# Optimization experiments

Hardware: AMD Instinct MI355X
Metric: run time of the kernel (lower is better)

## Reference

```python
import jax, jax.numpy as jnp
import numpy as np

DEPTH = 3  # chemprop default message passing depth


def setup_inputs() -> dict:
    key = jax.random.key(0)
    ks = jax.random.split(key, 10)
    n_atoms, n_bonds, max_nb, n_mols = 50000, 100000, 6, 2000
    atom_fdim, bond_fdim, hidden = 133, 147, 300
    f_atoms = jax.random.normal(ks[0], (n_atoms, atom_fdim), dtype=jnp.float32)
    f_bonds = jax.random.normal(ks[1], (n_bonds, bond_fdim), dtype=jnp.float32)
    a2b = jax.random.randint(ks[2], (n_atoms, max_nb), 0, n_bonds, dtype=jnp.int32)
    b2a = jax.random.randint(ks[3], (n_bonds,), 0, n_atoms, dtype=jnp.int32)
    b2revb = jax.random.randint(ks[4], (n_bonds,), 0, n_bonds, dtype=jnp.int32)
    mol_id = jnp.sort(jax.random.randint(ks[5], (n_atoms,), 0, n_mols, dtype=jnp.int32))
    W_i = jax.random.normal(ks[6], (bond_fdim, hidden), dtype=jnp.float32) * 0.05
    W_h = jax.random.normal(ks[7], (hidden, hidden), dtype=jnp.float32) * 0.05
    W_o = jax.random.normal(ks[8], (atom_fdim + hidden, hidden), dtype=jnp.float32) * 0.05
    b_o = jnp.zeros((hidden,), dtype=jnp.float32)
    return {"f_atoms": f_atoms, "f_bonds": f_bonds, "a2b": a2b, "b2a": b2a,
            "b2revb": b2revb, "mol_id": mol_id, "n_mols": n_mols,
            "W_i": W_i, "W_h": W_h, "W_o": W_o, "b_o": b_o}


def reference(f_atoms, f_bonds, a2b, b2a, b2revb, mol_id, n_mols, W_i, W_h, W_o, b_o):
    act = jax.nn.relu
    # W_i: bond features -> hidden; message init
    inp = f_bonds @ W_i                      # [n_bonds, h]
    message = act(inp)
    for _ in range(DEPTH - 1):
        nei = message[a2b]                    # [n_atoms, max_nb, h] gather
        a_message = nei.sum(axis=1)           # [n_atoms, h]
        rev = message[b2revb]                 # [n_bonds, h]
        message = a_message[b2a] - rev        # [n_bonds, h]
        message = act(inp + message @ W_h)
    # final atom readout
    a_message = message[a2b].sum(axis=1)      # [n_atoms, h]
    a_input = jnp.concatenate([f_atoms, a_message], axis=1)  # [n_atoms, fa+h]
    atom_hiddens = act(a_input @ W_o + b_o)   # [n_atoms, h]
    # ragged per-molecule mean (a_scope loop -> segment mean)
    sums = jax.ops.segment_sum(atom_hiddens, mol_id, num_segments=n_mols)
    counts = jax.ops.segment_sum(jnp.ones((atom_hiddens.shape[0],), dtype=atom_hiddens.dtype), mol_id, num_segments=n_mols)
    mol_vecs = jnp.where(counts[:, None] > 0, sums / jnp.maximum(counts, 1.0)[:, None], 0.0)
    return mol_vecs
```

## Files before the change

kernel.cpp:

```cpp
#include <hip/hip_runtime.h>
#include <cstddef>

#define H 300
#define RS 304
#define MAXNB 6
#define ASTR 312

typedef __attribute__((ext_vector_type(8)))  short bf16x8;
typedef __attribute__((ext_vector_type(16))) float f32x16;

__device__ __forceinline__ float bf2f(unsigned short u) {
    return __uint_as_float(((unsigned int)u) << 16);
}
__device__ __forceinline__ unsigned short f2bf(float f) {
    unsigned int u = __float_as_uint(f);
    u += 0x7FFFu + ((u >> 16) & 1u);
    return (unsigned short)(u >> 16);
}
__device__ __forceinline__ unsigned int sub2bf(unsigned int a, unsigned int b) {
    float d0 = bf2f((unsigned short)(a & 0xFFFFu)) - bf2f((unsigned short)(b & 0xFFFFu));
    float d1 = bf2f((unsigned short)(a >> 16))     - bf2f((unsigned short)(b >> 16));
    return (unsigned int)f2bf(d0) | ((unsigned int)f2bf(d1) << 16);
}
__device__ __forceinline__ unsigned int relu2(unsigned int w) {
    unsigned int r = w;
    if (w & 0x80000000u) r &= 0x0000FFFFu;
    if (w & 0x00008000u) r &= 0xFFFF0000u;
    return r;
}
__device__ __forceinline__ uint4 relu4(uint4 v) {
    v.x = relu2(v.x); v.y = relu2(v.y); v.z = relu2(v.z); v.w = relu2(v.w);
    return v;
}
__device__ __forceinline__ uint4 subpack4(uint4 a, uint4 b) {
    uint4 r;
    r.x = sub2bf(a.x, b.x); r.y = sub2bf(a.y, b.y);
    r.z = sub2bf(a.z, b.z); r.w = sub2bf(a.w, b.w);
    return r;
}


template<int S>
__global__ void __launch_bounds__(256)
pack_a_f32_c(const float* __restrict__ src, unsigned short* __restrict__ dst,
             int M, int K)
{
    __shared__ unsigned short sm[64 * 152];
    const int m0 = blockIdx.x * 64;
    const int r = threadIdx.x >> 2;
    const int q = threadIdx.x & 3;
    int mv = m0 + r; if (mv >= M) mv = M - 1;
    const float* rowF = src + (size_t)mv * K;
#pragma unroll
    for (int i = 0; i < (S * 4 + 3) / 4; ++i) {
        int c = q + i * 4;
        if (c * 4 < S * 16) {
            unsigned short h[4];
#pragma unroll
            for (int e = 0; e < 4; ++e) {
                int k = c * 4 + e;
                h[e] = (k < K) ? f2bf(rowF[k]) : (unsigned short)0;
            }
            uint2 o;
            o.x = (unsigned int)h[0] | ((unsigned int)h[1] << 16);
            o.y = (unsigned int)h[2] | ((unsigned int)h[3] << 16);
            *(uint2*)&sm[r * 152 + c * 4] = o;
        }
    }
    __syncthreads();
    for (int j = threadIdx.x; j < 2 * S * 64; j += 256) {
        int lane = j & 63;
        int t = j >> 6;
        int s = t % S;
        int mb2 = t / S;
        uint4 v = *(const uint4*)&sm[(mb2 * 32 + (lane & 31)) * 152 + s * 16 + (lane >> 5) * 8];
        int m_blk = blockIdx.x * 2 + mb2;
        *(uint4*)&dst[((size_t)(m_blk * S + s) * 64 + lane) * 8] = v;
    }
}

__global__ void __launch_bounds__(256)
pack_b(const float* __restrict__ src1, const float* __restrict__ src2,
       unsigned short* __restrict__ dst, int K1, int S1, int K2, int SB)
{
    int g = blockIdx.x * 256 + threadIdx.x;
    if (g >= 10 * SB * 64) return;
    int lane = g & 63;
    int t = g >> 6;
    int s = t % SB;
    int n_blk = t / SB;
    int n = n_blk * 32 + (lane & 31);
    unsigned int w[4];
#pragma unroll
    for (int p = 0; p < 4; ++p) {
        unsigned short h[2];
#pragma unroll
        for (int e = 0; e < 2; ++e) {
            int kf = s * 16 + (lane >> 5) * 8 + p * 2 + e;
            float v = 0.0f;
            if (n < H) {
                if (s < S1) {
                    if (kf < K1) v = src1[(size_t)kf * H + n];
                } else {
                    int k2 = kf - S1 * 16;
                    if (k2 < K2) v = src2[(size_t)k2 * H + n];
                }
            }
            h[e] = f2bf(v);
        }
        w[p] = (unsigned int)h[0] | ((unsigned int)h[1] << 16);
    }
    *(uint4*)&dst[(size_t)g * 8] = make_uint4(w[0], w[1], w[2], w[3]);
}

template<int RELU>
__global__ void __launch_bounds__(256)
aggregate_row(const unsigned short* __restrict__ msg, const int* __restrict__ a2b,
              unsigned short* __restrict__ amsg, int n_atoms)
{
    int gid = blockIdx.x * 256 + threadIdx.x;
    int total = n_atoms * 38;
    if (gid >= total) return;
    int atom = gid / 38;
    int g8 = gid - atom * 38;
    const int* nb = a2b + atom * MAXNB;
    float sum[8] = {};
#pragma unroll
    for (int j = 0; j < MAXNB; ++j) {
        int b = nb[j];
        uint4 v = *(const uint4*)&msg[(size_t)b * RS + g8 * 8];
        if (RELU) v = relu4(v);
        unsigned int ww[4] = {v.x, v.y, v.z, v.w};
#pragma unroll
        for (int p = 0; p < 4; ++p) {
            sum[p * 2]     += bf2f((unsigned short)(ww[p] & 0xFFFFu));
            sum[p * 2 + 1] += bf2f((unsigned short)(ww[p] >> 16));
        }
    }
    unsigned int ow[4];
#pragma unroll
    for (int p = 0; p < 4; ++p)
        ow[p] = (unsigned int)f2bf(sum[p * 2]) | ((unsigned int)f2bf(sum[p * 2 + 1]) << 16);
    *(uint4*)&amsg[(size_t)atom * RS + g8 * 8] = make_uint4(ow[0], ow[1], ow[2], ow[3]);
}

template<int S1, int S2, int SBL, int MODE, int RELUMSG>
__global__ void __launch_bounds__(640)
gemm_fused(const unsigned short* __restrict__ A1,
           const unsigned short* __restrict__ amsg,
           const unsigned short* __restrict__ msg,
           const int* __restrict__ b2a, const int* __restrict__ b2revb,
           const unsigned short* __restrict__ Bp,
           const float* __restrict__ bias,
           const unsigned short* __restrict__ inp_add,
           const float* __restrict__ Adense, int Kd,
           unsigned short* __restrict__ out, int M)
{
    __shared__ __align__(16) unsigned short smem[64 * ASTR];

    const int lane  = threadIdx.x & 63;
    const int w     = threadIdx.x >> 6;
    const int mrow  = lane & 31;
    const int quad  = lane >> 5;
    const int m0    = blockIdx.x * 64;

    if (threadIdx.x < 512) {
        const int r = threadIdx.x >> 3;
        const int q = threadIdx.x & 7;
        int mm = m0 + r;
        int mv = (mm < M) ? mm : 0;
        if (MODE == 0) {
            if (mm >= M) mv = M - 1;
            const float* rowF = Adense + (size_t)mv * Kd;
#pragma unroll
            for (int i = 0; i < 5; ++i) {
                int c = q + i * 8;
                if (c * 4 < S2 * 16) {
                    unsigned short h[4];
#pragma unroll
                    for (int e = 0; e < 4; ++e) {
                        int k = c * 4 + e;
                        h[e] = (k < Kd) ? f2bf(rowF[k]) : (unsigned short)0;
                    }
                    uint2 o;
                    o.x = (unsigned int)h[0] | ((unsigned int)h[1] << 16);
                    o.y = (unsigned int)h[2] | ((unsigned int)h[3] << 16);
                    *(uint2*)&smem[r * ASTR + c * 4] = o;
                }
            }
        } else {
            const unsigned short* rowA;
            const unsigned short* rowM = nullptr;
            if (MODE == 1) {
                rowA = amsg + (size_t)b2a[mv] * RS;
                rowM = msg  + (size_t)b2revb[mv] * RS;
            } else {
                rowA = amsg + (size_t)mv * RS;
            }
#pragma unroll
            for (int i = 0; i < 5; ++i) {
                int c = q + i * 8;
                if (c < 38) {
                    uint4 o;
                    if (MODE == 1) {
                        uint4 va = *(const uint4*)(rowA + c * 8);
                        uint4 vm = *(const uint4*)(rowM + c * 8);
                        if (RELUMSG) vm = relu4(vm);
                        o = subpack4(va, vm);
                    } else {
                        o = *(const uint4*)(rowA + c * 8);
                    }
                    *(uint4*)&smem[r * ASTR + c * 8] = o;
                }
            }
        }
    }
    __syncthreads();

    f32x16 acc_lo, acc_hi;
#pragma unroll
    for (int i = 0; i < 16; ++i) { acc_lo[i] = 0.0f; acc_hi[i] = 0.0f; }

    const unsigned short* pa1_lo = (S1 > 0)
        ? (A1 + ((size_t)(blockIdx.x * 2 + 0) * S1 * 64 + lane) * 8) : nullptr;
    const unsigned short* pa1_hi = (S1 > 0)
        ? (A1 + ((size_t)(blockIdx.x * 2 + 1) * S1 * 64 + lane) * 8) : nullptr;
    const unsigned short* pb = Bp + ((size_t)w * SBL * 64 + lane) * 8;

    constexpr int STOT = S1 + S2;

    auto loadA = [&](int s, const unsigned short* pa1x, int half) -> bf16x8 {
        if (s < S1) return *(const bf16x8*)(pa1x + (size_t)s * 512);
        return *(const bf16x8*)&smem[((half << 5) + mrow) * ASTR + (s - S1) * 16 + quad * 8];
    };

    bf16x8 b0, b1;
    b0 = *(const bf16x8*)(pb);
    if (STOT > 1) b1 = *(const bf16x8*)(pb + 512);

#pragma unroll
    for (int s = 0; s < STOT; s += 2) {
        bf16x8 a_lo = loadA(s, pa1_lo, 0);
        bf16x8 a_hi = loadA(s, pa1_hi, 1);
        acc_lo = __builtin_amdgcn_mfma_f32_32x32x16_bf16(a_lo, b0, acc_lo, 0, 0, 0);
        acc_hi = __builtin_amdgcn_mfma_f32_32x32x16_bf16(a_hi, b0, acc_hi, 0, 0, 0);
        if (s + 2 < STOT) b0 = *(const bf16x8*)(pb + (size_t)(s + 2) * 512);
        if (s + 1 < STOT) {
            bf16x8 a_lo2 = loadA(s + 1, pa1_lo, 0);
            bf16x8 a_hi2 = loadA(s + 1, pa1_hi, 1);
            acc_lo = __builtin_amdgcn_mfma_f32_32x32x16_bf16(a_lo2, b1, acc_lo, 0, 0, 0);
            acc_hi = __builtin_amdgcn_mfma_f32_32x32x16_bf16(a_hi2, b1, acc_hi, 0, 0, 0);
            if (s + 3 < STOT) b1 = *(const bf16x8*)(pb + (size_t)(s + 3) * 512);
        }
    }

    __syncthreads();

    {
        int col = w * 32 + mrow;
        if (col < 308) {
#pragma unroll
            for (int r = 0; r < 16; ++r) {
                int row = (r & 3) + 8 * (r >> 2) + 4 * quad;
                smem[row * 308 + col] = f2bf(acc_lo[r]);
            }
#pragma unroll
            for (int r = 0; r < 16; ++r) {
                int row = 32 + (r & 3) + 8 * (r >> 2) + 4 * quad;
                smem[row * 308 + col] = f2bf(acc_hi[r]);
            }
        }
    }
    __syncthreads();

    for (int idx = threadIdx.x; idx < 64 * 76; idx += 640) {
        int row = idx / 76, gcol = idx - row * 76;
        int mm = m0 + row;
        if (mm >= M) continue;
        int c0 = gcol * 4;
        uint2 raw = *(const uint2*)&smem[row * 308 + c0];
        uint2 o;
        if (MODE == 0) {
            o = raw;
        } else {
            unsigned short h[4] = {(unsigned short)(raw.x & 0xFFFFu), (unsigned short)(raw.x >> 16),
                                   (unsigned short)(raw.y & 0xFFFFu), (unsigned short)(raw.y >> 16)};
            float v[4];
#pragma unroll
            for (int e = 0; e < 4; ++e) v[e] = bf2f(h[e]);
            if (MODE == 1) {
                uint2 iv = *(const uint2*)&inp_add[(size_t)mm * RS + c0];
                v[0] += bf2f((unsigned short)(iv.x & 0xFFFFu));
                v[1] += bf2f((unsigned short)(iv.x >> 16));
                v[2] += bf2f((unsigned short)(iv.y & 0xFFFFu));
                v[3] += bf2f((unsigned short)(iv.y >> 16));
            } else {
#pragma unroll
                for (int e = 0; e < 4; ++e) v[e] += (c0 + e < H) ? bias[c0 + e] : 0.0f;
            }
#pragma unroll
            for (int e = 0; e < 4; ++e) h[e] = f2bf(fmaxf(v[e], 0.0f));
            o.x = (unsigned int)h[0] | ((unsigned int)h[1] << 16);
            o.y = (unsigned int)h[2] | ((unsigned int)h[3] << 16);
        }
        *(uint2*)&out[(size_t)mm * RS + c0] = o;
    }
}

__global__ void __launch_bounds__(128)
segmean_kernel(const unsigned short* __restrict__ ah,
               const int* __restrict__ mol_id, int n_atoms,
               float* __restrict__ out)
{
    int m = blockIdx.x;
    int lo = 0, hi = n_atoms;
    while (lo < hi) { int mid = (lo + hi) >> 1; if (mol_id[mid] < m) lo = mid + 1; else hi = mid; }
    int start = lo;
    hi = n_atoms;
    while (lo < hi) { int mid = (lo + hi) >> 1; if (mol_id[mid] < m + 1) lo = mid + 1; else hi = mid; }
    int end = lo;

    int c = threadIdx.x;
    float a0 = 0.f, a1 = 0.f, a2 = 0.f;
    for (int a = start; a < end; ++a) {
        const unsigned short* row = ah + (size_t)a * RS;
        a0 += bf2f(row[c]);
        a1 += bf2f(row[c + 128]);
        if (c < H - 256) a2 += bf2f(row[c + 256]);
    }
    float inv = (end > start) ? 1.0f / (float)(end - start) : 0.0f;
    float* orow = out + (size_t)m * H;
    orow[c] = a0 * inv;
    orow[c + 128] = a1 * inv;
    if (c < H - 256) orow[c + 256] = a2 * inv;
}

extern "C" void kernel_launch(void* const* d_in, const int* in_sizes, int n_in,
                              void* d_out, int out_size, void* d_ws, size_t ws_size,
                              hipStream_t stream)
{
    const float* f_atoms = (const float*)d_in[0];
    const float* f_bonds = (const float*)d_in[1];
    const int*   a2b     = (const int*)d_in[2];
    const int*   b2a     = (const int*)d_in[3];
    const int*   b2revb  = (const int*)d_in[4];
    const int*   mol_id  = (const int*)d_in[5];
    const float* W_i     = (const float*)d_in[7];
    const float* W_h     = (const float*)d_in[8];
    const float* W_o     = (const float*)d_in[9];
    const float* b_o     = (const float*)d_in[10];

    const int n_atoms   = in_sizes[5];
    const int n_bonds   = in_sizes[3];
    const int atom_fdim = in_sizes[0] / n_atoms;
    const int bond_fdim = in_sizes[1] / n_bonds;
    const int n_mols    = out_size / H;

    const int gAtoms  = (n_atoms + 63) / 64;
    const int gBonds  = (n_bonds + 63) / 64;

    const size_t bondsRS = (size_t)n_bonds * RS;
    const size_t atomsRS = (size_t)n_atoms * RS;
    const size_t wihSz   = 10 * 30 * 512;
    const size_t woSz    = 10 * 29 * 512;
    const size_t wh19Sz  = 10 * 19 * 512;

    unsigned short* inp  = (unsigned short*)d_ws;
    unsigned short* msgB = inp  + bondsRS;
    unsigned short* amsg = msgB + bondsRS;
    unsigned short* wih  = amsg + atomsRS;
    unsigned short* wo   = wih  + wihSz;
    unsigned short* wh19 = wo   + woSz;
    unsigned short* ah   = wh19 + wh19Sz;
    unsigned short* fap  = inp;

    dim3 blk(256);
    dim3 gblk(640);
    const int aggBlocks = (n_atoms * 38 + 255) / 256;

    pack_b<<<(10 * 30 * 64 + 255) / 256, blk, 0, stream>>>(W_i, W_h, wih, bond_fdim, 10, H, 30);
    pack_b<<<(10 * 19 * 64 + 255) / 256, blk, 0, stream>>>(W_h, W_h, wh19, H, 19, 0, 19);
    pack_b<<<(10 * 29 * 64 + 255) / 256, blk, 0, stream>>>(W_o, W_o + (size_t)atom_fdim * H, wo,
                                                           atom_fdim, 9, H, 29);

    gemm_fused<0, 10, 30, 0, 0><<<gBonds, gblk, 0, stream>>>(
        nullptr, nullptr, nullptr, nullptr, nullptr, wih, nullptr, nullptr,
        f_bonds, bond_fdim, inp, n_bonds);

    aggregate_row<1><<<aggBlocks, blk, 0, stream>>>(inp, a2b, amsg, n_atoms);
    gemm_fused<0, 19, 19, 1, 1><<<gBonds, gblk, 0, stream>>>(
        nullptr, amsg, inp, b2a, b2revb, wh19, nullptr, inp, nullptr, 0, msgB, n_bonds);

    aggregate_row<0><<<aggBlocks, blk, 0, stream>>>(msgB, a2b, amsg, n_atoms);
    gemm_fused<0, 19, 19, 1, 0><<<gBonds, gblk, 0, stream>>>(
        nullptr, amsg, msgB, b2a, b2revb, wh19, nullptr, inp, nullptr, 0, inp, n_bonds);

    aggregate_row<0><<<aggBlocks, blk, 0, stream>>>(inp, a2b, amsg, n_atoms);

    pack_a_f32_c<9><<<gAtoms, blk, 0, stream>>>(f_atoms, fap, n_atoms, atom_fdim);

    gemm_fused<9, 19, 29, 2, 0><<<gAtoms, gblk, 0, stream>>>(
        fap, amsg, nullptr, nullptr, nullptr, wo, b_o, nullptr, nullptr, 0, ah, n_atoms);

    segmean_kernel<<<n_mols, dim3(128), 0, stream>>>(ah, mol_id, n_atoms, (float*)d_out);
}
```

Baseline: 487.5 us.

## Split GEMM output columns across two blocks of 320 threads each

Each 64-row GEMM tile is now handled by two blocks of 5 waves, each computing half of the 300+ output columns, instead of one block of 10 waves. The goal is more, smaller blocks for better occupancy and load balance across CUs. The cost is that the A-tile staging (including the gathered amsg/msg rows and their subtraction in MODE 1) is done twice, once per block, which doubles that gather traffic and work.

```diff
diff --git a/kernel.cpp b/kernel.cpp
--- a/kernel.cpp
+++ b/kernel.cpp
@@ -5,6 +5,7 @@
 #define RS 304
 #define MAXNB 6
 #define ASTR 312
+#define CSTR 164
 
 typedef __attribute__((ext_vector_type(8)))  short bf16x8;
 typedef __attribute__((ext_vector_type(16))) float f32x16;
@@ -145,7 +146,7 @@
 }
 
 template<int S1, int S2, int SBL, int MODE, int RELUMSG>
-__global__ void __launch_bounds__(640)
+__global__ void __launch_bounds__(320)
 gemm_fused(const unsigned short* __restrict__ A1,
            const unsigned short* __restrict__ amsg,
            const unsigned short* __restrict__ msg,
@@ -162,19 +163,22 @@
     const int w     = threadIdx.x >> 6;
     const int mrow  = lane & 31;
     const int quad  = lane >> 5;
-    const int m0    = blockIdx.x * 64;
-
-    if (threadIdx.x < 512) {
-        const int r = threadIdx.x >> 3;
-        const int q = threadIdx.x & 7;
+    const int tile  = blockIdx.x >> 1;
+    const int nhalf = blockIdx.x & 1;
+    const int nbase = nhalf * 160;
+    const int m0    = tile * 64;
+
+    if (threadIdx.x < 256) {
+        const int r = threadIdx.x >> 2;
+        const int q = threadIdx.x & 3;
         int mm = m0 + r;
         int mv = (mm < M) ? mm : 0;
         if (MODE == 0) {
             if (mm >= M) mv = M - 1;
             const float* rowF = Adense + (size_t)mv * Kd;
 #pragma unroll
-            for (int i = 0; i < 5; ++i) {
-                int c = q + i * 8;
+            for (int i = 0; i < 10; ++i) {
+                int c = q + i * 4;
                 if (c * 4 < S2 * 16) {
                     unsigned short h[4];
 #pragma unroll
@@ -198,8 +202,8 @@
                 rowA = amsg + (size_t)mv * RS;
             }
 #pragma unroll
-            for (int i = 0; i < 5; ++i) {
-                int c = q + i * 8;
+            for (int i = 0; i < 10; ++i) {
+                int c = q + i * 4;
                 if (c < 38) {
                     uint4 o;
                     if (MODE == 1) {
@@ -222,10 +226,11 @@
     for (int i = 0; i < 16; ++i) { acc_lo[i] = 0.0f; acc_hi[i] = 0.0f; }
 
     const unsigned short* pa1_lo = (S1 > 0)
-        ? (A1 + ((size_t)(blockIdx.x * 2 + 0) * S1 * 64 + lane) * 8) : nullptr;
+        ? (A1 + ((size_t)(tile * 2 + 0) * S1 * 64 + lane) * 8) : nullptr;
     const unsigned short* pa1_hi = (S1 > 0)
-        ? (A1 + ((size_t)(blockIdx.x * 2 + 1) * S1 * 64 + lane) * 8) : nullptr;
-    const unsigned short* pb = Bp + ((size_t)w * SBL * 64 + lane) * 8;
+        ? (A1 + ((size_t)(tile * 2 + 1) * S1 * 64 + lane) * 8) : nullptr;
+    const int nblk = nhalf * 5 + w;
+    const unsigned short* pb = Bp + ((size_t)nblk * SBL * 64 + lane) * 8;
 
     constexpr int STOT = S1 + S2;
 
@@ -258,27 +263,27 @@
 
     {
         int col = w * 32 + mrow;
-        if (col < 308) {
-#pragma unroll
-            for (int r = 0; r < 16; ++r) {
-                int row = (r & 3) + 8 * (r >> 2) + 4 * quad;
-                smem[row * 308 + col] = f2bf(acc_lo[r]);
-            }
-#pragma unroll
-            for (int r = 0; r < 16; ++r) {
-                int row = 32 + (r & 3) + 8 * (r >> 2) + 4 * quad;
-                smem[row * 308 + col] = f2bf(acc_hi[r]);
-            }
+#pragma unroll
+        for (int r = 0; r < 16; ++r) {
+            int row = (r & 3) + 8 * (r >> 2) + 4 * quad;
+            smem[row * CSTR + col] = f2bf(acc_lo[r]);
+        }
+#pragma unroll
+        for (int r = 0; r < 16; ++r) {
+            int row = 32 + (r & 3) + 8 * (r >> 2) + 4 * quad;
+            smem[row * CSTR + col] = f2bf(acc_hi[r]);
         }
     }
     __syncthreads();
 
-    for (int idx = threadIdx.x; idx < 64 * 76; idx += 640) {
-        int row = idx / 76, gcol = idx - row * 76;
+    for (int idx = threadIdx.x; idx < 64 * 40; idx += 320) {
+        int row = idx / 40, chunk = idx - row * 40;
+        if (nhalf == 1 && chunk >= 36) continue;
         int mm = m0 + row;
         if (mm >= M) continue;
-        int c0 = gcol * 4;
-        uint2 raw = *(const uint2*)&smem[row * 308 + c0];
+        int c0l = chunk * 4;
+        int c0g = nbase + c0l;
+        uint2 raw = *(const uint2*)&smem[row * CSTR + c0l];
         uint2 o;
         if (MODE == 0) {
             o = raw;
@@ -289,21 +294,21 @@
 #pragma unroll
             for (int e = 0; e < 4; ++e) v[e] = bf2f(h[e]);
             if (MODE == 1) {
-                uint2 iv = *(const uint2*)&inp_add[(size_t)mm * RS + c0];
+                uint2 iv = *(const uint2*)&inp_add[(size_t)mm * RS + c0g];
                 v[0] += bf2f((unsigned short)(iv.x & 0xFFFFu));
                 v[1] += bf2f((unsigned short)(iv.x >> 16));
                 v[2] += bf2f((unsigned short)(iv.y & 0xFFFFu));
                 v[3] += bf2f((unsigned short)(iv.y >> 16));
             } else {
 #pragma unroll
-                for (int e = 0; e < 4; ++e) v[e] += (c0 + e < H) ? bias[c0 + e] : 0.0f;
+                for (int e = 0; e < 4; ++e) v[e] += (c0g + e < H) ? bias[c0g + e] : 0.0f;
             }
 #pragma unroll
             for (int e = 0; e < 4; ++e) h[e] = f2bf(fmaxf(v[e], 0.0f));
             o.x = (unsigned int)h[0] | ((unsigned int)h[1] << 16);
             o.y = (unsigned int)h[2] | ((unsigned int)h[3] << 16);
         }
-        *(uint2*)&out[(size_t)mm * RS + c0] = o;
+        *(uint2*)&out[(size_t)mm * RS + c0g] = o;
     }
 }
 
@@ -358,6 +363,8 @@
 
     const int gAtoms  = (n_atoms + 63) / 64;
     const int gBonds  = (n_bonds + 63) / 64;
+    const int gB2     = gBonds * 2;
+    const int gA2     = gAtoms * 2;
 
     const size_t bondsRS = (size_t)n_bonds * RS;
     const size_t atomsRS = (size_t)n_atoms * RS;
@@ -375,7 +382,7 @@
     unsigned short* fap  = inp;
 
     dim3 blk(256);
-    dim3 gblk(640);
+    dim3 gblk(320);
     const int aggBlocks = (n_atoms * 38 + 255) / 256;
 
     pack_b<<<(10 * 30 * 64 + 255) / 256, blk, 0, stream>>>(W_i, W_h, wih, bond_fdim, 10, H, 30);
@@ -383,23 +390,23 @@
     pack_b<<<(10 * 29 * 64 + 255) / 256, blk, 0, stream>>>(W_o, W_o + (size_t)atom_fdim * H, wo,
                                                            atom_fdim, 9, H, 29);
 
-    gemm_fused<0, 10, 30, 0, 0><<<gBonds, gblk, 0, stream>>>(
+    gemm_fused<0, 10, 30, 0, 0><<<gB2, gblk, 0, stream>>>(
         nullptr, nullptr, nullptr, nullptr, nullptr, wih, nullptr, nullptr,
         f_bonds, bond_fdim, inp, n_bonds);
 
     aggregate_row<1><<<aggBlocks, blk, 0, stream>>>(inp, a2b, amsg, n_atoms);
-    gemm_fused<0, 19, 19, 1, 1><<<gBonds, gblk, 0, stream>>>(
+    gemm_fused<0, 19, 19, 1, 1><<<gB2, gblk, 0, stream>>>(
         nullptr, amsg, inp, b2a, b2revb, wh19, nullptr, inp, nullptr, 0, msgB, n_bonds);
 
     aggregate_row<0><<<aggBlocks, blk, 0, stream>>>(msgB, a2b, amsg, n_atoms);
-    gemm_fused<0, 19, 19, 1, 0><<<gBonds, gblk, 0, stream>>>(
+    gemm_fused<0, 19, 19, 1, 0><<<gB2, gblk, 0, stream>>>(
         nullptr, amsg, msgB, b2a, b2revb, wh19, nullptr, inp, nullptr, 0, inp, n_bonds);
 
     aggregate_row<0><<<aggBlocks, blk, 0, stream>>>(inp, a2b, amsg, n_atoms);
 
     pack_a_f32_c<9><<<gAtoms, blk, 0, stream>>>(f_atoms, fap, n_atoms, atom_fdim);
 
-    gemm_fused<9, 19, 29, 2, 0><<<gAtoms, gblk, 0, stream>>>(
+    gemm_fused<9, 19, 29, 2, 0><<<gA2, gblk, 0, stream>>>(
         fap, amsg, nullptr, nullptr, nullptr, wo, b_o, nullptr, nullptr, 0, ah, n_atoms);
 
     segmean_kernel<<<n_mols, dim3(128), 0, stream>>>(ah, mol_id, n_atoms, (float*)d_out);
```

Result: slower. 586.4 us (+20.3%).
